# Optimization experiments

Hardware: AMD Instinct MI355X
Metric: run time of the kernel (lower is better)

## Reference

```python
import jax, jax.numpy as jnp
import numpy as np

D = 2048      # hidden_size
S = 2048      # seq_len (batch packed, batch=1)
H = 16        # num_attention_heads
QL = 1536     # q_lora_rank
KVL = 512     # kv_lora_rank (latent dim, also v head size)
DN = 128      # qk_nope_head_dim
DR = 64       # qk_rope_head_dim
DV = 128      # v_head_dim
I = 8192      # mlp intermediate
EPS = 1e-6
SCALE = (DN + DR) ** -0.5  # softmax_scale = q_head_dim**-0.5 (no yarn mscale)


def rmsnorm(x, w):
    return x * jax.lax.rsqrt(jnp.mean(x * x, axis=-1, keepdims=True) + EPS) * w


def rotate_half(x):
    h = x.shape[-1] // 2
    return jnp.concatenate([-x[..., h:], x[..., :h]], axis=-1)


def setup_inputs() -> dict:
    key = jax.random.key(0)
    ks = jax.random.split(key, 10)
    s = 0.02
    # real RoPE tables (rotate_half layout)
    inv_freq = 1.0 / (10000.0 ** (jnp.arange(0, DR, 2, dtype=jnp.float32) / DR))
    t = jnp.arange(S, dtype=jnp.float32)
    emb = jnp.concatenate([jnp.outer(t, inv_freq)] * 2, axis=-1)  # [S, DR]
    return {
        'hidden_states': jax.random.normal(ks[0], (1, S, D), dtype=jnp.float32),
        'cos': jnp.cos(emb),
        'sin': jnp.sin(emb),
        'ln1_w': jnp.ones((D,), jnp.float32),
        'q_a_w': jax.random.normal(ks[1], (D, QL)) * s,
        'q_a_ln_w': jnp.ones((QL,), jnp.float32),
        'q_b_w': jax.random.normal(ks[2], (QL, H * (DN + DR))) * s,
        'kv_a_w': jax.random.normal(ks[3], (D, KVL + DR)) * s,
        'kv_a_ln_w': jnp.ones((KVL,), jnp.float32),
        'kc_w': jax.random.normal(ks[4], (H, DN, KVL)) * s,
        'vc_w': jax.random.normal(ks[5], (H, KVL, DV)) * s,
        'o_w': jax.random.normal(ks[6], (H * DV, D)) * s,
        'ln2_w': jnp.ones((D,), jnp.float32),
        'gate_up_w': jax.random.normal(ks[7], (D, 2 * I)) * s,
        'down_w': jax.random.normal(ks[8], (I, D)) * s,
    }


def reference(hidden_states, cos, sin, ln1_w, q_a_w, q_a_ln_w, q_b_w,
              kv_a_w, kv_a_ln_w, kc_w, vc_w, o_w, ln2_w, gate_up_w, down_w):
    residual = hidden_states
    h = rmsnorm(hidden_states, ln1_w)[0]                      # [S, D]
    # --- Q path: low-rank down + RMSNorm + up, split nope/rope ---
    q = rmsnorm(h @ q_a_w, q_a_ln_w) @ q_b_w                  # [S, H*(DN+DR)]
    q = q.reshape(S, H, DN + DR)
    q_nope, q_pe = q[..., :DN], q[..., DN:]
    # kc BMM: absorb W_UK, project q_nope into latent dim     # [S, H, KVL]
    q_lat = jnp.einsum('shd,hdc->shc', q_nope, kc_w)
    # --- KV path: compressed latent + shared rope key ---
    kv = h @ kv_a_w                                           # [S, KVL+DR]
    k_lat = rmsnorm(kv[:, :KVL], kv_a_ln_w)                   # [S, KVL] (also V)
    k_pe = kv[:, KVL:]                                        # [S, DR]
    # --- RoPE on the rope split only ---
    q_pe = q_pe * cos[:, None, :] + rotate_half(q_pe) * sin[:, None, :]
    k_pe = k_pe * cos + rotate_half(k_pe) * sin
    # --- latent MQA attention: q/k dim = KVL+DR, v dim = KVL ---
    qf = jnp.concatenate([q_lat, q_pe], axis=-1)              # [S, H, KVL+DR]
    kf = jnp.concatenate([k_lat, k_pe], axis=-1)              # [S, KVL+DR]
    scores = jnp.einsum('shc,tc->hst', qf, kf) * SCALE        # [H, S, S]
    causal = jnp.tril(jnp.ones((S, S), dtype=bool))
    scores = jnp.where(causal, scores, jnp.float32(-1e30))
    attn = jax.nn.softmax(scores, axis=-1)
    o_lat = jnp.einsum('hst,tc->shc', attn, k_lat)            # [S, H, KVL]
    # vc BMM: latent -> v_head_dim
    o = jnp.einsum('shc,hcv->shv', o_lat, vc_w).reshape(S, H * DV)
    attn_out = (o @ o_w)[None]                                # [1, S, D]
    hidden = residual + attn_out
    # --- dense SwiGLU MLP ---
    x2 = rmsnorm(hidden, ln2_w)
    gu = x2 @ gate_up_w
    mlp = (jax.nn.silu(gu[..., :I]) * gu[..., I:]) @ down_w
    return hidden + mlp
```

## Files before the change

### kernel.cpp

```cpp
#include <hip/hip_runtime.h>
#include <stdint.h>


#define S_   2048
#define D_   2048
#define H_   16
#define QL_  1536
#define KVL_ 512
#define DN_  128
#define DR_  64
#define DV_  128
#define I_   8192
#define SCALE_ 0.07216878364870323f

typedef __bf16 bf16x8 __attribute__((ext_vector_type(8)));
typedef float f32x4 __attribute__((ext_vector_type(4)));

__device__ __forceinline__ unsigned short f2bf(float f) {
  unsigned int u = __builtin_bit_cast(unsigned int, f);
  u += 0x7fffu + ((u >> 16) & 1u);
  return (unsigned short)(u >> 16);
}
__device__ __forceinline__ float bf2f(unsigned short b) {
  unsigned int u = ((unsigned int)b) << 16;
  return __builtin_bit_cast(float, u);
}

__device__ __forceinline__ float block_sum256(float v) {
  __shared__ float red[4];
  #pragma unroll
  for (int o = 32; o; o >>= 1) v += __shfl_xor(v, o);
  __syncthreads();
  if ((threadIdx.x & 63) == 0) red[threadIdx.x >> 6] = v;
  __syncthreads();
  return red[0] + red[1] + red[2] + red[3];
}
__device__ __forceinline__ float block_max256(float v) {
  __shared__ float red[4];
  #pragma unroll
  for (int o = 32; o; o >>= 1) v = fmaxf(v, __shfl_xor(v, o));
  __syncthreads();
  if ((threadIdx.x & 63) == 0) red[threadIdx.x >> 6] = v;
  __syncthreads();
  return fmaxf(fmaxf(red[0], red[1]), fmaxf(red[2], red[3]));
}

__device__ __forceinline__ void gload_lds16(const void* g, void* l) {
  void* gn = const_cast<void*>(g);
  __builtin_amdgcn_global_load_lds(
      (__attribute__((address_space(1))) void*)gn,
      (__attribute__((address_space(3))) void*)l, 16, 0, 0);
}

template <int OUT, int ADD_RES, int TRI, int CK>
__global__ __launch_bounds__(256) void gemm_bt(
    const unsigned short* __restrict__ A, const unsigned short* __restrict__ Bt,
    void* __restrict__ C, const float* __restrict__ R, float scale,
    int M, int N, int K, int lda, int ldb, int ldc,
    long sA, long sB, long sC) {
  __shared__ unsigned short As[128 * 64];
  __shared__ unsigned short Bs[128 * 64];
  const int b = blockIdx.z;
  int bx = blockIdx.x, by = blockIdx.y;
  if (TRI) {
    const int t = blockIdx.x;
    int i = (int)((sqrtf(8.f * t + 1.f) - 1.f) * 0.5f);
    while ((i + 1) * (i + 2) / 2 <= t) ++i;
    while (i * (i + 1) / 2 > t) --i;
    by = i;
    bx = t - i * (i + 1) / 2;
  }
  const int m0 = by * 128, n0 = bx * 128;
  if (CK) K = min(K, m0 + 128);
  const int tid = threadIdx.x, w = tid >> 6, lane = tid & 63;
  const int wm = (w >> 1) * 64, wn = (w & 1) * 64;
  const int fr = lane & 15;
  const int fq = lane >> 4;
  const int sr = lane >> 3;
  const int sch = (lane & 7) ^ sr;
  const unsigned short* Ab = A + (long)b * sA;
  const unsigned short* Bb = Bt + (long)b * sB;
  long aOff[4], bOff[4];
  #pragma unroll
  for (int i = 0; i < 4; ++i) {
    const int row = w * 32 + i * 8 + sr;
    aOff[i] = (long)(m0 + row) * lda + sch * 8;
    bOff[i] = (long)(n0 + row) * ldb + sch * 8;
  }
  const int ca0 = fq ^ (fr & 7);
  const int ca1 = (4 + fq) ^ (fr & 7);

  f32x4 acc[4][4] = {};

  for (int k0 = 0; k0 < K; k0 += 64) {
    #pragma unroll
    for (int i = 0; i < 4; ++i) {
      gload_lds16(Ab + aOff[i] + k0, As + (w * 32 + i * 8) * 64);
      gload_lds16(Bb + bOff[i] + k0, Bs + (w * 32 + i * 8) * 64);
    }
    __syncthreads();
    #pragma unroll
    for (int s = 0; s < 2; ++s) {
      const int cc = s ? ca1 : ca0;
      bf16x8 af[4], bf[4];
      #pragma unroll
      for (int i = 0; i < 4; ++i)
        af[i] = *(const bf16x8*)(As + (wm + i * 16 + fr) * 64 + cc * 8);
      #pragma unroll
      for (int j = 0; j < 4; ++j)
        bf[j] = *(const bf16x8*)(Bs + (wn + j * 16 + fr) * 64 + cc * 8);
      #pragma unroll
      for (int i = 0; i < 4; ++i)
        #pragma unroll
        for (int j = 0; j < 4; ++j)
          acc[i][j] = __builtin_amdgcn_mfma_f32_16x16x32_bf16(af[i], bf[j],
                                                              acc[i][j], 0, 0, 0);
    }
    __syncthreads();
  }

  const long cb = (long)b * sC;
  #pragma unroll
  for (int i = 0; i < 4; ++i) {
    const int row0 = m0 + wm + i * 16 + fq * 4;
    #pragma unroll
    for (int j = 0; j < 4; ++j) {
      const int col = n0 + wn + j * 16 + fr;
      #pragma unroll
      for (int r = 0; r < 4; ++r) {
        float v = acc[i][j][r] * scale;
        if (OUT == 2) {
          const float o = __shfl_xor(v, 1);
          const float res = v / (1.f + __expf(-v)) * o;
          if (((fr & 1) == 0) && col < N)
            ((unsigned short*)C)[cb + (long)(row0 + r) * ldc + (col >> 1)] =
                f2bf(res);
        } else {
          if (col < N) {
            const long idx = cb + (long)(row0 + r) * ldc + col;
            float vv = v;
            if (ADD_RES) vv += R[idx];
            if (OUT == 1) ((unsigned short*)C)[idx] = f2bf(vv);
            else          ((float*)C)[idx] = vv;
          }
        }
      }
    }
  }
}

__global__ void transpose_f2b(const float* __restrict__ in,
                              unsigned short* __restrict__ out, int Rr, int Cc,
                              long sIn, long sOut) {
  const int b = blockIdx.z;
  in += (long)b * sIn;
  out += (long)b * sOut;
  __shared__ float t[32][33];
  const int c0 = blockIdx.x * 32, r0 = blockIdx.y * 32;
  const int tx = threadIdx.x, ty = threadIdx.y;
  #pragma unroll
  for (int i = 0; i < 4; ++i)
    t[ty + i * 8][tx] = in[(long)(r0 + ty + i * 8) * Cc + c0 + tx];
  __syncthreads();
  #pragma unroll
  for (int i = 0; i < 4; ++i)
    out[(long)(c0 + ty + i * 8) * Rr + r0 + tx] = f2bf(t[tx][ty + i * 8]);
}

__global__ void transpose_f2b_ilv(const float* __restrict__ in,
                                  unsigned short* __restrict__ out) {
  __shared__ float t[32][33];
  const int c0 = blockIdx.x * 32, r0 = blockIdx.y * 32;
  const int tx = threadIdx.x, ty = threadIdx.y;
  #pragma unroll
  for (int i = 0; i < 4; ++i)
    t[ty + i * 8][tx] = in[(long)(r0 + ty + i * 8) * (2 * I_) + c0 + tx];
  __syncthreads();
  #pragma unroll
  for (int i = 0; i < 4; ++i) {
    const int c = c0 + ty + i * 8;
    const int n = ((c & (I_ - 1)) << 1) | (c >> 13);
    out[(long)n * D_ + r0 + tx] = f2bf(t[tx][ty + i * 8]);
  }
}

__global__ void rmsnorm_k(const float* __restrict__ x, const float* __restrict__ w,
                          unsigned short* __restrict__ y, int C) {
  const int row = blockIdx.x, tid = threadIdx.x;
  const float* xr = x + (long)row * C;
  float ss = 0.f;
  for (int c = tid; c < C; c += 256) { float v = xr[c]; ss += v * v; }
  ss = block_sum256(ss);
  const float rms = rsqrtf(ss / C + 1e-6f);
  for (int c = tid; c < C; c += 256)
    y[(long)row * C + c] = f2bf(xr[c] * rms * w[c]);
}

__global__ void q_post(const float* __restrict__ q, const float* __restrict__ cs,
                       const float* __restrict__ sn, unsigned short* __restrict__ qnope,
                       unsigned short* __restrict__ qf) {
  const int s = blockIdx.x, tid = threadIdx.x;
  const float* qr = q + (long)s * 3072;
  for (int c = tid; c < 3072; c += 256) {
    const int h = c / 192, d = c % 192;
    if (d < 128) {
      qnope[(long)s * 2048 + h * 128 + d] = f2bf(qr[c]);
    } else {
      const int j = d - 128;
      const float x = qr[c];
      const float rot = (j < 32) ? -qr[h * 192 + 128 + j + 32]
                                 :  qr[h * 192 + 128 + j - 32];
      const float v = x * cs[s * 64 + j] + rot * sn[s * 64 + j];
      qf[(long)h * (S_ * 576) + (long)s * 576 + 512 + j] = f2bf(v);
    }
  }
}

__global__ void kv_post(const float* __restrict__ kv, const float* __restrict__ w,
                        const float* __restrict__ cs, const float* __restrict__ sn,
                        unsigned short* __restrict__ kf, unsigned short* __restrict__ klt) {
  const int s = blockIdx.x, tid = threadIdx.x;
  const float* kr = kv + (long)s * 576;
  float ss = 0.f;
  for (int c = tid; c < 512; c += 256) { float v = kr[c]; ss += v * v; }
  ss = block_sum256(ss);
  const float rms = rsqrtf(ss / 512.f + 1e-6f);
  for (int c = tid; c < 576; c += 256) {
    if (c < 512) {
      const float v = kr[c] * rms * w[c];
      const unsigned short bv = f2bf(v);
      kf[(long)s * 576 + c] = bv;
      klt[(long)c * S_ + s] = bv;
    } else {
      const int j = c - 512;
      const float x = kr[c];
      const float rot = (j < 32) ? -kr[512 + j + 32] : kr[512 + j - 32];
      kf[(long)s * 576 + c] = f2bf(x * cs[s * 64 + j] + rot * sn[s * 64 + j]);
    }
  }
}

__global__ void softmax_causal_ip(unsigned short* __restrict__ sc, long hstride) {
  const int row = blockIdx.x, tid = threadIdx.x;
  unsigned short* sr = sc + (long)blockIdx.z * hstride + (long)row * S_;
  const int n = row + 1;
  const int kmax = ((row >> 7) + 1) << 7;
  float mx = -1e30f;
  for (int c = tid; c < n; c += 256) mx = fmaxf(mx, bf2f(sr[c]));
  mx = block_max256(mx);
  float e[8];
  float sum = 0.f;
  #pragma unroll
  for (int k = 0; k < 8; ++k) {
    const int c = tid + k * 256;
    if (c < n) { e[k] = __expf(bf2f(sr[c]) - mx); sum += e[k]; }
  }
  sum = block_sum256(sum);
  const float inv = 1.f / sum;
  #pragma unroll
  for (int k = 0; k < 8; ++k) {
    const int c = tid + k * 256;
    if (c < n) sr[c] = f2bf(e[k] * inv);
    else if (c < kmax) sr[c] = 0;
  }
}

extern "C" void kernel_launch(void* const* d_in, const int* in_sizes, int n_in,
                              void* d_out, int out_size, void* d_ws, size_t ws_size,
                              hipStream_t stream) {
  const float* hs   = (const float*)d_in[0];
  const float* cs   = (const float*)d_in[1];
  const float* sn   = (const float*)d_in[2];
  const float* ln1  = (const float*)d_in[3];
  const float* qaw  = (const float*)d_in[4];
  const float* qaln = (const float*)d_in[5];
  const float* qbw  = (const float*)d_in[6];
  const float* kvaw = (const float*)d_in[7];
  const float* kvln = (const float*)d_in[8];
  const float* kcw  = (const float*)d_in[9];
  const float* vcw  = (const float*)d_in[10];
  const float* ow   = (const float*)d_in[11];
  const float* ln2  = (const float*)d_in[12];
  const float* guw  = (const float*)d_in[13];
  const float* dww  = (const float*)d_in[14];
  float* out = (float*)d_out;
  char* ws = (char*)d_ws;

  unsigned short* hbf   = (unsigned short*)(ws + 0);
  float*          qa    = (float*)(ws + 8388608);
  unsigned short* qan   = (unsigned short*)(ws + 20971520);
  float*          q     = (float*)(ws + 27262976);
  unsigned short* qnope = (unsigned short*)(ws + 52428800);
  unsigned short* sc    = (unsigned short*)(ws + 0);
  unsigned short* qf    = (unsigned short*)(ws + 67108864);
  float*          kv    = (float*)(ws + 104857600);
  unsigned short* kf    = (unsigned short*)(ws + 109576192);
  unsigned short* klt   = (unsigned short*)(ws + 111935488);
  unsigned short* wt2   = (unsigned short*)(ws + 114032640);
  unsigned short* wt    = (unsigned short*)(ws + 116129792);
  unsigned short* olat  = (unsigned short*)(ws + 116129792);
  unsigned short* obf   = (unsigned short*)(ws + 0);
  float*          hidden= (float*)(ws + 8388608);
  unsigned short* x2    = (unsigned short*)(ws + 25165824);
  unsigned short* mlp   = (unsigned short*)(ws + 33554432);

  const dim3 B256(256), Bt32(32, 8);

  rmsnorm_k<<<S_, B256, 0, stream>>>(hs, ln1, hbf, D_);
  transpose_f2b<<<dim3(QL_/32, D_/32, 1), Bt32, 0, stream>>>(qaw, wt, D_, QL_, 0, 0);
  gemm_bt<0,0,0,0><<<dim3(QL_/128, S_/128, 1), B256, 0, stream>>>(
      hbf, wt, qa, nullptr, 1.f, S_, QL_, D_, D_, D_, QL_, 0, 0, 0);
  rmsnorm_k<<<S_, B256, 0, stream>>>(qa, qaln, qan, QL_);
  transpose_f2b<<<dim3(3072/32, QL_/32, 1), Bt32, 0, stream>>>(qbw, wt, QL_, 3072, 0, 0);
  gemm_bt<0,0,0,0><<<dim3(3072/128, S_/128, 1), B256, 0, stream>>>(
      qan, wt, q, nullptr, 1.f, S_, 3072, QL_, QL_, QL_, 3072, 0, 0, 0);
  q_post<<<S_, B256, 0, stream>>>(q, cs, sn, qnope, qf);
  transpose_f2b<<<dim3(576/32, D_/32, 1), Bt32, 0, stream>>>(kvaw, wt, D_, 576, 0, 0);
  gemm_bt<0,0,0,0><<<dim3(5, S_/128, 1), B256, 0, stream>>>(
      hbf, wt, kv, nullptr, 1.f, S_, 576, D_, D_, D_, 576, 0, 0, 0);
  kv_post<<<S_, B256, 0, stream>>>(kv, kvln, cs, sn, kf, klt);
  transpose_f2b<<<dim3(512/32, 128/32, H_), Bt32, 0, stream>>>(kcw, wt, 128, 512, 65536, 65536);
  transpose_f2b<<<dim3(128/32, 512/32, H_), Bt32, 0, stream>>>(vcw, wt2, 512, 128, 65536, 65536);
  gemm_bt<1,0,0,0><<<dim3(4, S_/128, H_), B256, 0, stream>>>(
      qnope, wt, qf, nullptr, 1.f, S_, 512, 128, 2048, 128, 576,
      128, 65536, (long)S_ * 576);
  for (int g = 0; g < 2; ++g) {
    const unsigned short* qfg = qf + (long)g * 8 * S_ * 576;
    gemm_bt<1,0,1,0><<<dim3(136, 1, 8), B256, 0, stream>>>(
        qfg, kf, sc, nullptr, SCALE_, S_, S_, 576, 576, 576, S_,
        (long)S_ * 576, 0, (long)S_ * S_);
    softmax_causal_ip<<<dim3(S_, 1, 8), B256, 0, stream>>>(sc, (long)S_ * S_);
    gemm_bt<1,0,0,1><<<dim3(4, 16, 8), B256, 0, stream>>>(
        sc, klt, olat + (long)g * 8 * S_ * 512, nullptr, 1.f,
        S_, 512, S_, S_, S_, 512, (long)S_ * S_, 0, (long)S_ * 512);
  }
  gemm_bt<1,0,0,0><<<dim3(1, S_/128, H_), B256, 0, stream>>>(
      olat, wt2, obf, nullptr, 1.f, S_, 128, 512, 512, 512, 2048,
      (long)S_ * 512, 65536, 128);
  transpose_f2b<<<dim3(D_/32, D_/32, 1), Bt32, 0, stream>>>(ow, wt, D_, D_, 0, 0);
  gemm_bt<0,1,0,0><<<dim3(D_/128, S_/128, 1), B256, 0, stream>>>(
      obf, wt, hidden, hs, 1.f, S_, D_, D_, D_, D_, D_, 0, 0, 0);
  rmsnorm_k<<<S_, B256, 0, stream>>>(hidden, ln2, x2, D_);
  transpose_f2b_ilv<<<dim3(2 * I_ / 32, D_/32, 1), Bt32, 0, stream>>>(guw, wt);
  gemm_bt<2,0,0,0><<<dim3(2 * I_ / 128, S_/128, 1), B256, 0, stream>>>(
      x2, wt, mlp, nullptr, 1.f, S_, 2 * I_, D_, D_, D_, I_, 0, 0, 0);
  transpose_f2b<<<dim3(D_/32, I_/32, 1), Bt32, 0, stream>>>(dww, wt, I_, D_, 0, 0);
  gemm_bt<0,1,0,0><<<dim3(D_/128, S_/128, 1), B256, 0, stream>>>(
      mlp, wt, out, hidden, 1.f, S_, D_, I_, I_, I_, D_, 0, 0, 0);
}
```

Baseline: 1.081 ms.

## Load B operand fragments directly from global memory into registers, bypassing LDS

The GEMM kernel stops staging the B tile in shared memory. Each wave now loads its MFMA B fragments straight from global memory into registers, half before the barrier and half after it. This halves LDS usage and removes the B LDS reads. In exchange, waves that share the same B columns reload them redundantly from global memory (each B row is read by two waves), and loads are less coalesced, with 16-byte chunks strided by ldb.

Result: slower. 1.451 ms (+34.3%).

```diff
diff --git a/kernel.cpp b/kernel.cpp
--- a/kernel.cpp
+++ b/kernel.cpp
@@ -59,7 +59,6 @@
     int M, int N, int K, int lda, int ldb, int ldc,
     long sA, long sB, long sC) {
   __shared__ unsigned short As[128 * 64];
-  __shared__ unsigned short Bs[128 * 64];
   const int b = blockIdx.z;
   int bx = blockIdx.x, by = blockIdx.y;
   if (TRI) {
@@ -80,13 +79,14 @@
   const int sch = (lane & 7) ^ sr;
   const unsigned short* Ab = A + (long)b * sA;
   const unsigned short* Bb = Bt + (long)b * sB;
-  long aOff[4], bOff[4];
-  #pragma unroll
-  for (int i = 0; i < 4; ++i) {
-    const int row = w * 32 + i * 8 + sr;
-    aOff[i] = (long)(m0 + row) * lda + sch * 8;
-    bOff[i] = (long)(n0 + row) * ldb + sch * 8;
-  }
+  long aOff[4];
+  #pragma unroll
+  for (int i = 0; i < 4; ++i)
+    aOff[i] = (long)(m0 + w * 32 + i * 8 + sr) * lda + sch * 8;
+  const unsigned short* bPtr[4];
+  #pragma unroll
+  for (int j = 0; j < 4; ++j)
+    bPtr[j] = Bb + (long)(n0 + wn + j * 16 + fr) * ldb + fq * 8;
   const int ca0 = fq ^ (fr & 7);
   const int ca1 = (4 + fq) ^ (fr & 7);
 
@@ -94,28 +94,36 @@
 
   for (int k0 = 0; k0 < K; k0 += 64) {
     #pragma unroll
-    for (int i = 0; i < 4; ++i) {
+    for (int i = 0; i < 4; ++i)
       gload_lds16(Ab + aOff[i] + k0, As + (w * 32 + i * 8) * 64);
-      gload_lds16(Bb + bOff[i] + k0, Bs + (w * 32 + i * 8) * 64);
-    }
+    bf16x8 b0[4];
+    #pragma unroll
+    for (int j = 0; j < 4; ++j)
+      b0[j] = *(const bf16x8*)(bPtr[j] + k0);
     __syncthreads();
-    #pragma unroll
-    for (int s = 0; s < 2; ++s) {
-      const int cc = s ? ca1 : ca0;
-      bf16x8 af[4], bf[4];
-      #pragma unroll
-      for (int i = 0; i < 4; ++i)
-        af[i] = *(const bf16x8*)(As + (wm + i * 16 + fr) * 64 + cc * 8);
+    bf16x8 b1[4];
+    #pragma unroll
+    for (int j = 0; j < 4; ++j)
+      b1[j] = *(const bf16x8*)(bPtr[j] + k0 + 32);
+    bf16x8 af[4];
+    #pragma unroll
+    for (int i = 0; i < 4; ++i)
+      af[i] = *(const bf16x8*)(As + (wm + i * 16 + fr) * 64 + ca0 * 8);
+    #pragma unroll
+    for (int i = 0; i < 4; ++i)
       #pragma unroll
       for (int j = 0; j < 4; ++j)
-        bf[j] = *(const bf16x8*)(Bs + (wn + j * 16 + fr) * 64 + cc * 8);
+        acc[i][j] = __builtin_amdgcn_mfma_f32_16x16x32_bf16(af[i], b0[j],
+                                                            acc[i][j], 0, 0, 0);
+    #pragma unroll
+    for (int i = 0; i < 4; ++i)
+      af[i] = *(const bf16x8*)(As + (wm + i * 16 + fr) * 64 + ca1 * 8);
+    #pragma unroll
+    for (int i = 0; i < 4; ++i)
       #pragma unroll
-      for (int i = 0; i < 4; ++i)
-        #pragma unroll
-        for (int j = 0; j < 4; ++j)
-          acc[i][j] = __builtin_amdgcn_mfma_f32_16x16x32_bf16(af[i], bf[j],
-                                                              acc[i][j], 0, 0, 0);
-    }
+      for (int j = 0; j < 4; ++j)
+        acc[i][j] = __builtin_amdgcn_mfma_f32_16x16x32_bf16(af[i], b1[j],
+                                                            acc[i][j], 0, 0, 0);
     __syncthreads();
   }
 
```
